# Kernel tuning notes

Hardware: AMD Instinct MI355X
Metric: run time of the kernel (lower is better)

Reference implementation:

```python
import jax, jax.numpy as jnp
import numpy as np

EMBED_DIM = 1024
NUM_HEADS = 16
HEAD_DIM = EMBED_DIM // NUM_HEADS
B, S = 4, 2048


def setup_inputs() -> dict:
    key = jax.random.key(0)
    ks = jax.random.split(key, 9)
    scale = 1.0 / np.sqrt(EMBED_DIM)
    inp = {
        "inputs": jax.random.normal(ks[0], (B, S, EMBED_DIM), dtype=jnp.float32),
        "rotation_params": jax.random.normal(ks[1], (B, S, EMBED_DIM), dtype=jnp.float32),
        "entangle_params": jax.random.normal(ks[2], (B, S, EMBED_DIM), dtype=jnp.float32),
        # Linear weights stored as (out, in) like torch; applied as x @ W.T
        "Wq": jax.random.normal(ks[3], (EMBED_DIM, EMBED_DIM), dtype=jnp.float32) * scale,
        "Wk": jax.random.normal(ks[4], (EMBED_DIM, EMBED_DIM), dtype=jnp.float32) * scale,
        "Wv": jax.random.normal(ks[5], (EMBED_DIM, EMBED_DIM), dtype=jnp.float32) * scale,
        "Wrot": jax.random.normal(ks[6], (EMBED_DIM, EMBED_DIM), dtype=jnp.float32) * scale,
        "Went": jax.random.normal(ks[7], (EMBED_DIM, EMBED_DIM), dtype=jnp.float32) * scale,
        "Wo": jax.random.normal(ks[8], (EMBED_DIM, EMBED_DIM), dtype=jnp.float32) * scale,
    }
    return inp


def _split_heads(x):
    b, s, e = x.shape
    return x.reshape(b, s, NUM_HEADS, HEAD_DIM).transpose(0, 2, 1, 3)  # (B,H,S,D)


def reference(inputs, rotation_params, entangle_params, Wq, Wk, Wv, Wrot, Went, Wo):
    Q = inputs @ Wq.T + rotation_params @ Wrot.T
    K = inputs @ Wk.T + entangle_params @ Went.T
    V = inputs @ Wv.T
    Qh, Kh, Vh = _split_heads(Q), _split_heads(K), _split_heads(V)
    scores = jnp.einsum("bhqd,bhkd->bhqk", Qh, Kh) / jnp.sqrt(jnp.float32(HEAD_DIM))
    attn = jax.nn.softmax(scores, axis=-1)  # dropout p=0 -> identity
    out = jnp.einsum("bhqk,bhkd->bhqd", attn, Vh)
    out = out.transpose(0, 2, 1, 3).reshape(inputs.shape[0], inputs.shape[1], EMBED_DIM)
    return out @ Wo.T
```

## Files before the change

### kernel.cpp

```cpp
#include <hip/hip_runtime.h>
#include <stdint.h>


typedef unsigned short u16;
typedef __bf16 bf16x8 __attribute__((ext_vector_type(8)));
typedef float f32x4 __attribute__((ext_vector_type(4)));
typedef float f32x16 __attribute__((ext_vector_type(16)));
typedef uint32_t u32x4 __attribute__((ext_vector_type(4)));

#define MFMA_BF16(a, b, c) __builtin_amdgcn_mfma_f32_16x16x32_bf16((a), (b), (c), 0, 0, 0)
#define MFMA32(a, b, c)    __builtin_amdgcn_mfma_f32_32x32x16_bf16((a), (b), (c), 0, 0, 0)
#define GAMMA 0.18033688011112042f
#define BHSTRIDE 131072
#define FENCE() __builtin_amdgcn_sched_barrier(0)

static __device__ __forceinline__ u16 f2bf(float f) {
    uint32_t u = __builtin_bit_cast(uint32_t, f);
    u = (u + 0x7FFFu + ((u >> 16) & 1u)) >> 16;
    return (u16)u;
}

static __device__ __forceinline__ uint32_t pk_rne2(float a, float b) {
    uint32_t ua = __builtin_bit_cast(uint32_t, a);
    uint32_t ub = __builtin_bit_cast(uint32_t, b);
    ua += 0x7FFFu + ((ua >> 16) & 1u);
    ub += 0x7FFFu + ((ub >> 16) & 1u);
    return __builtin_amdgcn_perm(ub, ua, 0x07060302);
}

static __device__ __forceinline__ void async_copy16(const void* g, void* l) {
    __builtin_amdgcn_global_load_lds((__attribute__((address_space(1))) void*)g,
                                     (__attribute__((address_space(3))) void*)l,
                                     16, 0, 0);
}

static __device__ __forceinline__ float aexp2(float x) {
    float r;
    asm("v_exp_f32 %0, %1" : "=v"(r) : "v"(x));
    return r;
}

static __device__ __forceinline__ uint32_t cvtpk(float a, float b) {
    uint32_t r;
    asm("v_cvt_pk_bf16_f32 %0, %1, %2" : "=v"(r) : "v"(a), "v"(b));
    return r;
}

static __device__ __forceinline__ void plswap(uint32_t& a, uint32_t& b) {
    asm("v_permlane32_swap_b32 %0, %1" : "+v"(a), "+v"(b));
}

static __device__ __forceinline__ bf16x8 mkfrag(uint32_t w0, uint32_t w1,
                                                uint32_t w2, uint32_t w3) {
    u32x4 u = {w0, w1, w2, w3};
    return __builtin_bit_cast(bf16x8, u);
}

struct CvtArgs { const float* s[6]; u16* d[6]; };

__global__ __launch_bounds__(256) void cvt_kernel(CvtArgs a, int nelem) {
    const float* s = a.s[blockIdx.z];
    u16* d = a.d[blockIdx.z];
    int i = (blockIdx.x * 256 + threadIdx.x) * 8;
    float4 f0 = *(const float4*)(s + i);
    float4 f1 = *(const float4*)(s + i + 4);
    uint4 w;
    w.x = pk_rne2(f0.x, f0.y); w.y = pk_rne2(f0.z, f0.w);
    w.z = pk_rne2(f1.x, f1.y); w.w = pk_rne2(f1.z, f1.w);
    *(uint4*)(d + i) = w;
}

__global__ __launch_bounds__(256, 3) void qk_proj(
    const u16* __restrict__ Xb,
    const u16* __restrict__ Wqb, const u16* __restrict__ RVb,
    const u16* __restrict__ Wrotb, u16* __restrict__ Qhm,
    const u16* __restrict__ Wkb, const u16* __restrict__ EOb,
    const u16* __restrict__ Wentb, u16* __restrict__ Khm)
{
    __shared__ __align__(16) u16 lA[128 * 64];
    __shared__ __align__(16) u16 lB[128 * 64];

    const int tid  = threadIdx.x;
    const int lane = tid & 63;
    const int wave = tid >> 6;
    const int wm   = (wave >> 1) * 64;
    const int wn   = (wave & 1) * 64;
    const size_t m0 = (size_t)blockIdx.x * 128;

    const bool isK = blockIdx.y >= 8;
    const size_t n0 = (size_t)(blockIdx.y & 7) * 128;
    const u16* A0 = Xb;
    const u16* W0 = isK ? Wkb  : Wqb;
    const u16* A1 = isK ? EOb  : RVb;
    const u16* W1 = isK ? Wentb : Wrotb;
    u16*       C  = isK ? Khm  : Qhm;
    const float scale = isK ? 1.0f : GAMMA;

    const int row8 = tid >> 3;
    const int cp   = tid & 7;
    const int fr   = lane & 15;
    const int g    = lane >> 4;

    f32x4 acc[4][4] = {};

    for (int p = 0; p < 2; ++p) {
        const u16* A = p ? A1 : A0;
        const u16* W = p ? W1 : W0;
        for (int k0 = 0; k0 < 1024; k0 += 64) {
            __syncthreads();
#pragma unroll
            for (int it = 0; it < 4; ++it) {
                int row = it * 32 + row8;
                int sc = cp ^ (((row >> 3) ^ row) & 7);
                async_copy16(A + ((m0 + row) * 1024 + k0 + sc * 8),
                             (char*)lA + it * 4096 + tid * 16);
                async_copy16(W + ((n0 + row) * 1024 + k0 + sc * 8),
                             (char*)lB + it * 4096 + tid * 16);
            }
            __syncthreads();

            bf16x8 af[4][2], bfm[4][2];
#pragma unroll
            for (int i = 0; i < 4; ++i) {
                int row = wm + i * 16 + fr;
                int sw = ((row >> 3) ^ row) & 7;
                af[i][0] = *(const bf16x8*)(lA + row * 64 + (g ^ sw) * 8);
                af[i][1] = *(const bf16x8*)(lA + row * 64 + ((4 + g) ^ sw) * 8);
            }
#pragma unroll
            for (int j = 0; j < 4; ++j) {
                int row = wn + j * 16 + fr;
                int sw = ((row >> 3) ^ row) & 7;
                bfm[j][0] = *(const bf16x8*)(lB + row * 64 + (g ^ sw) * 8);
                bfm[j][1] = *(const bf16x8*)(lB + row * 64 + ((4 + g) ^ sw) * 8);
            }
#pragma unroll
            for (int i = 0; i < 4; ++i)
#pragma unroll
                for (int j = 0; j < 4; ++j) {
                    acc[i][j] = MFMA_BF16(af[i][0], bfm[j][0], acc[i][j]);
                    acc[i][j] = MFMA_BF16(af[i][1], bfm[j][1], acc[i][j]);
                }
        }
    }

#pragma unroll
    for (int i = 0; i < 4; ++i)
#pragma unroll
        for (int j = 0; j < 4; ++j)
#pragma unroll
            for (int rg = 0; rg < 4; ++rg) {
                size_t row = m0 + wm + i * 16 + g * 4 + rg;
                size_t col = n0 + wn + j * 16 + fr;
                size_t addr = ((row >> 11) * 16 + (col >> 6)) * BHSTRIDE
                            + (row & 2047) * 64 + (col & 63);
                C[addr] = f2bf(acc[i][j][rg] * scale);
            }
}

template <int AMODE, int CMODE>
__global__ __launch_bounds__(256, 2) void gemm_bt(
    const u16* __restrict__ A0, const u16* __restrict__ W0,
    const u16* __restrict__ A1, const u16* __restrict__ W1,
    void* __restrict__ Cv, int K, int npairs, float scale)
{
    __shared__ __align__(16) u16 lA[128 * 64];
    __shared__ __align__(16) u16 lB[128 * 64];

    const int tid  = threadIdx.x;
    const int lane = tid & 63;
    const int wave = tid >> 6;
    const int wm   = (wave >> 1) * 64;
    const int wn   = (wave & 1) * 64;
    const size_t m0 = (size_t)blockIdx.x * 128;
    const size_t n0 = (size_t)blockIdx.y * 128;

    const int row8 = tid >> 3;
    const int cp   = tid & 7;
    const int fr   = lane & 15;
    const int g    = lane >> 4;

    const size_t bb = (m0 >> 11) * 16;
    const size_t s0 = m0 & 2047;

    f32x4 acc[4][4] = {};

    for (int p = 0; p < npairs; ++p) {
        const u16* A = p ? A1 : A0;
        const u16* W = p ? W1 : W0;
        for (int k0 = 0; k0 < K; k0 += 64) {
            __syncthreads();
#pragma unroll
            for (int it = 0; it < 4; ++it) {
                int row = it * 32 + row8;
                int sc = cp ^ (((row >> 3) ^ row) & 7);
                if (AMODE == 0) {
                    async_copy16(A + ((m0 + row) * (size_t)K + k0 + sc * 8),
                                 (char*)lA + it * 4096 + tid * 16);
                } else {
                    size_t base = (bb + (size_t)(k0 >> 6)) * BHSTRIDE;
                    async_copy16(A + base + (s0 + row) * 64 + sc * 8,
                                 (char*)lA + it * 4096 + tid * 16);
                }
                async_copy16(W + ((n0 + row) * (size_t)K + k0 + sc * 8),
                             (char*)lB + it * 4096 + tid * 16);
            }
            __syncthreads();

            bf16x8 af[4][2], bfm[4][2];
#pragma unroll
            for (int i = 0; i < 4; ++i) {
                int row = wm + i * 16 + fr;
                int sw = ((row >> 3) ^ row) & 7;
                af[i][0] = *(const bf16x8*)(lA + row * 64 + (g ^ sw) * 8);
                af[i][1] = *(const bf16x8*)(lA + row * 64 + ((4 + g) ^ sw) * 8);
            }
#pragma unroll
            for (int j = 0; j < 4; ++j) {
                int row = wn + j * 16 + fr;
                int sw = ((row >> 3) ^ row) & 7;
                bfm[j][0] = *(const bf16x8*)(lB + row * 64 + (g ^ sw) * 8);
                bfm[j][1] = *(const bf16x8*)(lB + row * 64 + ((4 + g) ^ sw) * 8);
            }
#pragma unroll
            for (int i = 0; i < 4; ++i)
#pragma unroll
                for (int j = 0; j < 4; ++j) {
                    acc[i][j] = MFMA_BF16(af[i][0], bfm[j][0], acc[i][j]);
                    acc[i][j] = MFMA_BF16(af[i][1], bfm[j][1], acc[i][j]);
                }
        }
    }

#pragma unroll
    for (int i = 0; i < 4; ++i)
#pragma unroll
        for (int j = 0; j < 4; ++j) {
            if (CMODE == 2) {
                size_t row0 = m0 + wm + i * 16 + g * 4;
                size_t col  = n0 + wn + j * 16 + fr;
                size_t addr = ((row0 >> 11) * 16 + (col >> 6)) * BHSTRIDE
                            + (size_t)(col & 63) * 2048 + (row0 & 2047);
                ushort4 pk;
                pk.x = f2bf(acc[i][j][0] * scale);
                pk.y = f2bf(acc[i][j][1] * scale);
                pk.z = f2bf(acc[i][j][2] * scale);
                pk.w = f2bf(acc[i][j][3] * scale);
                *(ushort4*)((u16*)Cv + addr) = pk;
            } else {
#pragma unroll
                for (int rg = 0; rg < 4; ++rg) {
                    size_t row = m0 + wm + i * 16 + g * 4 + rg;
                    size_t col = n0 + wn + j * 16 + fr;
                    float v = acc[i][j][rg] * scale;
                    if (CMODE == 0) {
                        ((float*)Cv)[row * 1024 + col] = v;
                    } else {
                        size_t addr = ((row >> 11) * 16 + (col >> 6)) * BHSTRIDE
                                    + (row & 2047) * 64 + (col & 63);
                        ((u16*)Cv)[addr] = f2bf(v);
                    }
                }
            }
        }
}

__global__ __launch_bounds__(256, 2) void flash_kernel(
    const u16* __restrict__ Qhm, const u16* __restrict__ Khm,
    const u16* __restrict__ Vt, u16* __restrict__ Ohm)
{
    __shared__ __align__(16) u16 sK[2][128 * 64];
    __shared__ __align__(16) u16 sVt[2][64 * 128];

    const int tid  = threadIdx.x;
    const int lane = tid & 63;
    const int wave = tid >> 6;
    const int l31  = lane & 31;
    const int hg   = lane >> 5;

    const int lin  = blockIdx.x;
    const int slot = lin >> 3;
    const int bh   = (lin & 7) + 8 * (slot >> 3);
    const int q0   = (slot & 7) * 256;

    const u16* Qh = Qhm + (size_t)bh * BHSTRIDE;
    const u16* Kh = Khm + (size_t)bh * BHSTRIDE;
    const u16* Vh = Vt  + (size_t)bh * BHSTRIDE;
    u16*       Oh = Ohm + (size_t)bh * BHSTRIDE;

    bf16x8 qbf[2][4];
#pragma unroll
    for (int qt = 0; qt < 2; ++qt)
#pragma unroll
        for (int dc = 0; dc < 4; ++dc)
            qbf[qt][dc] = *(const bf16x8*)(Qh +
                (size_t)(q0 + wave * 64 + qt * 32 + l31) * 64 + dc * 16 + hg * 8);

    f32x16 oaccA[2] = {};
    f32x16 oaccB[2] = {};
    float lsA[2] = {}, lsB[2] = {};

    const int krow8 = tid >> 3, kcp = tid & 7;
    const int vd16  = tid >> 4, vcp = tid & 15;

    auto stage = [&](int buf, int kt) {
#pragma unroll
        for (int it = 0; it < 4; ++it) {
            int row = it * 32 + krow8;
            int sc = kcp ^ (((row >> 3) ^ row) & 7);
            async_copy16(Kh + (size_t)(kt * 128 + row) * 64 + sc * 8,
                         (char*)(&sK[buf][0]) + it * 4096 + tid * 16);
        }
#pragma unroll
        for (int it = 0; it < 4; ++it) {
            int d = it * 16 + vd16;
            int sc = vcp ^ (d & 15);
            async_copy16(Vh + (size_t)d * 2048 + kt * 128 + sc * 8,
                         (char*)(&sVt[buf][0]) + it * 4096 + tid * 16);
        }
    };

    auto qk2 = [&](const u16* sKc, int kc, f32x16& sa0, f32x16& sa1) {
        sa0 = (f32x16){};
        sa1 = (f32x16){};
        const int krow = kc * 32 + l31;
        const int ksw = ((krow >> 3) ^ krow) & 7;
#pragma unroll
        for (int dc = 0; dc < 4; ++dc) {
            bf16x8 ka = *(const bf16x8*)(sKc + krow * 64 + ((dc * 2 + hg) ^ ksw) * 8);
            sa0 = MFMA32(ka, qbf[0][dc], sa0);
            sa1 = MFMA32(ka, qbf[1][dc], sa1);
        }
    };

    auto sm = [&](const f32x16& sa, bf16x8& o0, bf16x8& o1, float* ls) {
        float p[16];
#pragma unroll
        for (int r = 0; r < 16; ++r) p[r] = aexp2(sa[r]);
#pragma unroll
        for (int r = 0; r < 16; ++r) ls[r & 1] += p[r];
        uint32_t w0 = cvtpk(p[0],  p[1]),  w1 = cvtpk(p[2],  p[3]);
        uint32_t w2 = cvtpk(p[4],  p[5]),  w3 = cvtpk(p[6],  p[7]);
        uint32_t w4 = cvtpk(p[8],  p[9]),  w5 = cvtpk(p[10], p[11]);
        uint32_t w6 = cvtpk(p[12], p[13]), w7 = cvtpk(p[14], p[15]);
        plswap(w0, w2); plswap(w1, w3);
        plswap(w4, w6); plswap(w5, w7);
        o0 = mkfrag(w0, w1, w2, w3);
        o1 = mkfrag(w4, w5, w6, w7);
    };

    auto pv2 = [&](const u16* sVc, int kc, bf16x8 a0, bf16x8 a1,
                   bf16x8 b0, bf16x8 b1) {
        bf16x8 vb[2][2];
#pragma unroll
        for (int sub = 0; sub < 2; ++sub)
#pragma unroll
            for (int dt = 0; dt < 2; ++dt) {
                int dr = dt * 32 + l31;
                vb[sub][dt] = *(const bf16x8*)(sVc + dr * 128 +
                    ((kc * 4 + sub * 2 + hg) ^ (dr & 15)) * 8);
            }
        oaccA[0] = MFMA32(a0, vb[0][0], oaccA[0]);
        oaccA[1] = MFMA32(a0, vb[0][1], oaccA[1]);
        oaccB[0] = MFMA32(b0, vb[0][0], oaccB[0]);
        oaccB[1] = MFMA32(b0, vb[0][1], oaccB[1]);
        oaccA[0] = MFMA32(a1, vb[1][0], oaccA[0]);
        oaccA[1] = MFMA32(a1, vb[1][1], oaccA[1]);
        oaccB[0] = MFMA32(b1, vb[1][0], oaccB[0]);
        oaccB[1] = MFMA32(b1, vb[1][1], oaccB[1]);
    };

    stage(0, 0);
    __syncthreads();

    int cur = 0;
    for (int kt = 0; kt < 16; ++kt) {
        const u16* sKc = &sK[cur][0];
        const u16* sVc = &sVt[cur][0];

        f32x16 sA, sB, nA, nB;
        qk2(sKc, 0, sA, sB);
        if (kt < 15) stage(cur ^ 1, kt + 1);
        FENCE();

        bf16x8 a0, a1, b0, b1;
        sm(sA, a0, a1, lsA);   FENCE();
        qk2(sKc, 1, nA, nB);   FENCE();
        sm(sB, b0, b1, lsB);   FENCE();
        pv2(sVc, 0, a0, a1, b0, b1); FENCE();
        sm(nA, a0, a1, lsA);   FENCE();
        qk2(sKc, 2, sA, sB);   FENCE();
        sm(nB, b0, b1, lsB);   FENCE();
        pv2(sVc, 1, a0, a1, b0, b1); FENCE();
        sm(sA, a0, a1, lsA);   FENCE();
        qk2(sKc, 3, nA, nB);   FENCE();
        sm(sB, b0, b1, lsB);   FENCE();
        pv2(sVc, 2, a0, a1, b0, b1); FENCE();
        sm(nA, a0, a1, lsA);   FENCE();
        sm(nB, b0, b1, lsB);   FENCE();
        pv2(sVc, 3, a0, a1, b0, b1);

        __syncthreads();
        cur ^= 1;
    }

#pragma unroll
    for (int qt = 0; qt < 2; ++qt) {
        float l = qt ? (lsB[0] + lsB[1]) : (lsA[0] + lsA[1]);
        l += __shfl_xor(l, 32);
        float inv = 1.0f / l;
        const f32x16* oa = qt ? oaccB : oaccA;
#pragma unroll
        for (int r = 0; r < 16; ++r) {
            int row = (r & 3) + 4 * hg + 8 * (r >> 2);
            float invr = __shfl(inv, row);
            size_t grow = (size_t)q0 + wave * 64 + qt * 32 + row;
            Oh[grow * 64 + l31]      = f2bf(oa[0][r] * invr);
            Oh[grow * 64 + 32 + l31] = f2bf(oa[1][r] * invr);
        }
    }
}

extern "C" void kernel_launch(void* const* d_in, const int* in_sizes, int n_in,
                              void* d_out, int out_size, void* d_ws, size_t ws_size,
                              hipStream_t stream)
{
    const float* X    = (const float*)d_in[0];
    const float* R    = (const float*)d_in[1];
    const float* E    = (const float*)d_in[2];
    const float* Wq   = (const float*)d_in[3];
    const float* Wk   = (const float*)d_in[4];
    const float* Wv   = (const float*)d_in[5];
    const float* Wrot = (const float*)d_in[6];
    const float* Went = (const float*)d_in[7];
    const float* Wo   = (const float*)d_in[8];

    const size_t NT = 8192 * 1024;
    const size_t NW = 1024 * 1024;

    u16* Qhm = (u16*)d_out;
    u16* Khm = Qhm + NT;
    u16* Xb  = (u16*)d_ws;
    u16* RVb = Xb + NT;
    u16* EOb = RVb + NT;
    u16* Wqb = EOb + NT;
    u16* Wkb   = Wqb + NW;
    u16* Wvb   = Wkb + NW;
    u16* Wrotb = Wvb + NW;
    u16* Wentb = Wrotb + NW;
    u16* Wob   = Wentb + NW;

    {
        CvtArgs a{};
        a.s[0] = X; a.s[1] = R; a.s[2] = E;
        a.d[0] = Xb; a.d[1] = RVb; a.d[2] = EOb;
        cvt_kernel<<<dim3(4096, 1, 3), 256, 0, stream>>>(a, (int)NT);
    }
    {
        CvtArgs a{};
        a.s[0] = Wq; a.s[1] = Wk; a.s[2] = Wv; a.s[3] = Wrot; a.s[4] = Went; a.s[5] = Wo;
        a.d[0] = Wqb; a.d[1] = Wkb; a.d[2] = Wvb; a.d[3] = Wrotb; a.d[4] = Wentb; a.d[5] = Wob;
        cvt_kernel<<<dim3(512, 1, 6), 256, 0, stream>>>(a, (int)NW);
    }

    qk_proj<<<dim3(64, 16), 256, 0, stream>>>(Xb, Wqb, RVb, Wrotb, Qhm,
                                              Wkb, EOb, Wentb, Khm);
    gemm_bt<0, 2><<<dim3(64, 8), 256, 0, stream>>>(Xb, Wvb, nullptr, nullptr,
                                                   RVb, 1024, 1, 1.0f);
    flash_kernel<<<dim3(512), 256, 0, stream>>>(Qhm, Khm, RVb, EOb);
    gemm_bt<1, 0><<<dim3(64, 8), 256, 0, stream>>>(EOb, Wob, nullptr, nullptr,
                                                   d_out, 1024, 1, 1.0f);
}
```

Measured before the change: 364.1 us.

## Fuse V projection into QK projection kernel and merge conversion launches

Merges the two fp32-to-bf16 conversion launches into a single 9-slice launch, where weight slices exit early past their size. Adds a qkv_proj kernel that computes Q, K and V projections in one grid of 64x24 blocks, writing V transposed into a separate workspace region. The new path runs only when the workspace is large enough, so V no longer overwrites RVb. This removes launch overhead and tail gaps between kernels, at the cost of load imbalance because V blocks do half the K-loop work.

```diff
diff --git a/kernel.cpp b/kernel.cpp
--- a/kernel.cpp
+++ b/kernel.cpp
@@ -56,9 +56,10 @@
     return __builtin_bit_cast(bf16x8, u);
 }
 
-struct CvtArgs { const float* s[6]; u16* d[6]; };
-
-__global__ __launch_bounds__(256) void cvt_kernel(CvtArgs a, int nelem) {
+struct CvtArgs { const float* s[9]; u16* d[9]; };
+
+__global__ __launch_bounds__(256) void cvt_kernel(CvtArgs a) {
+    if (blockIdx.z >= 3 && blockIdx.x >= 512) return;
     const float* s = a.s[blockIdx.z];
     u16* d = a.d[blockIdx.z];
     int i = (blockIdx.x * 256 + threadIdx.x) * 8;
@@ -70,6 +71,113 @@
     *(uint4*)(d + i) = w;
 }
 
+__global__ __launch_bounds__(256, 3) void qkv_proj(
+    const u16* __restrict__ Xb,
+    const u16* __restrict__ Wqb, const u16* __restrict__ RVb,
+    const u16* __restrict__ Wrotb, u16* __restrict__ Qhm,
+    const u16* __restrict__ Wkb, const u16* __restrict__ EOb,
+    const u16* __restrict__ Wentb, u16* __restrict__ Khm,
+    const u16* __restrict__ Wvb, u16* __restrict__ Vt)
+{
+    __shared__ __align__(16) u16 lA[128 * 64];
+    __shared__ __align__(16) u16 lB[128 * 64];
+
+    const int tid  = threadIdx.x;
+    const int lane = tid & 63;
+    const int wave = tid >> 6;
+    const int wm   = (wave >> 1) * 64;
+    const int wn   = (wave & 1) * 64;
+    const size_t m0 = (size_t)blockIdx.x * 128;
+
+    const int sel = blockIdx.y >> 3;
+    const size_t n0 = (size_t)(blockIdx.y & 7) * 128;
+    const u16* W0 = sel == 0 ? Wqb : (sel == 1 ? Wkb : Wvb);
+    const u16* A1 = sel == 1 ? EOb : RVb;
+    const u16* W1 = sel == 1 ? Wentb : Wrotb;
+    const float scale = sel == 0 ? GAMMA : 1.0f;
+    const int npairs = sel == 2 ? 1 : 2;
+
+    const int row8 = tid >> 3;
+    const int cp   = tid & 7;
+    const int fr   = lane & 15;
+    const int g    = lane >> 4;
+
+    f32x4 acc[4][4] = {};
+
+    for (int p = 0; p < npairs; ++p) {
+        const u16* A = p ? A1 : Xb;
+        const u16* W = p ? W1 : W0;
+        for (int k0 = 0; k0 < 1024; k0 += 64) {
+            __syncthreads();
+#pragma unroll
+            for (int it = 0; it < 4; ++it) {
+                int row = it * 32 + row8;
+                int sc = cp ^ (((row >> 3) ^ row) & 7);
+                async_copy16(A + ((m0 + row) * 1024 + k0 + sc * 8),
+                             (char*)lA + it * 4096 + tid * 16);
+                async_copy16(W + ((n0 + row) * 1024 + k0 + sc * 8),
+                             (char*)lB + it * 4096 + tid * 16);
+            }
+            __syncthreads();
+
+            bf16x8 af[4][2], bfm[4][2];
+#pragma unroll
+            for (int i = 0; i < 4; ++i) {
+                int row = wm + i * 16 + fr;
+                int sw = ((row >> 3) ^ row) & 7;
+                af[i][0] = *(const bf16x8*)(lA + row * 64 + (g ^ sw) * 8);
+                af[i][1] = *(const bf16x8*)(lA + row * 64 + ((4 + g) ^ sw) * 8);
+            }
+#pragma unroll
+            for (int j = 0; j < 4; ++j) {
+                int row = wn + j * 16 + fr;
+                int sw = ((row >> 3) ^ row) & 7;
+                bfm[j][0] = *(const bf16x8*)(lB + row * 64 + (g ^ sw) * 8);
+                bfm[j][1] = *(const bf16x8*)(lB + row * 64 + ((4 + g) ^ sw) * 8);
+            }
+#pragma unroll
+            for (int i = 0; i < 4; ++i)
+#pragma unroll
+                for (int j = 0; j < 4; ++j) {
+                    acc[i][j] = MFMA_BF16(af[i][0], bfm[j][0], acc[i][j]);
+                    acc[i][j] = MFMA_BF16(af[i][1], bfm[j][1], acc[i][j]);
+                }
+        }
+    }
+
+    if (sel == 2) {
+#pragma unroll
+        for (int i = 0; i < 4; ++i)
+#pragma unroll
+            for (int j = 0; j < 4; ++j) {
+                size_t row0 = m0 + wm + i * 16 + g * 4;
+                size_t col  = n0 + wn + j * 16 + fr;
+                size_t addr = ((row0 >> 11) * 16 + (col >> 6)) * BHSTRIDE
+                            + (size_t)(col & 63) * 2048 + (row0 & 2047);
+                ushort4 pk;
+                pk.x = f2bf(acc[i][j][0]);
+                pk.y = f2bf(acc[i][j][1]);
+                pk.z = f2bf(acc[i][j][2]);
+                pk.w = f2bf(acc[i][j][3]);
+                *(ushort4*)(Vt + addr) = pk;
+            }
+    } else {
+        u16* C = sel == 0 ? Qhm : Khm;
+#pragma unroll
+        for (int i = 0; i < 4; ++i)
+#pragma unroll
+            for (int j = 0; j < 4; ++j)
+#pragma unroll
+                for (int rg = 0; rg < 4; ++rg) {
+                    size_t row = m0 + wm + i * 16 + g * 4 + rg;
+                    size_t col = n0 + wn + j * 16 + fr;
+                    size_t addr = ((row >> 11) * 16 + (col >> 6)) * BHSTRIDE
+                                + (row & 2047) * 64 + (col & 63);
+                    C[addr] = f2bf(acc[i][j][rg] * scale);
+                }
+    }
+}
+
 __global__ __launch_bounds__(256, 3) void qk_proj(
     const u16* __restrict__ Xb,
     const u16* __restrict__ Wqb, const u16* __restrict__ RVb,
@@ -89,7 +197,6 @@
 
     const bool isK = blockIdx.y >= 8;
     const size_t n0 = (size_t)(blockIdx.y & 7) * 128;
-    const u16* A0 = Xb;
     const u16* W0 = isK ? Wkb  : Wqb;
     const u16* A1 = isK ? EOb  : RVb;
     const u16* W1 = isK ? Wentb : Wrotb;
@@ -104,7 +211,7 @@
     f32x4 acc[4][4] = {};
 
     for (int p = 0; p < 2; ++p) {
-        const u16* A = p ? A1 : A0;
+        const u16* A = p ? A1 : Xb;
         const u16* W = p ? W1 : W0;
         for (int k0 = 0; k0 < 1024; k0 += 64) {
             __syncthreads();
@@ -449,25 +556,33 @@
     u16* Wrotb = Wvb + NW;
     u16* Wentb = Wrotb + NW;
     u16* Wob   = Wentb + NW;
+    u16* VtX   = Wob + NW;
+
+    const bool bigws = ws_size >= (4 * NT + 6 * NW) * sizeof(u16);
+    u16* Vt = bigws ? VtX : RVb;
 
     {
         CvtArgs a{};
-        a.s[0] = X; a.s[1] = R; a.s[2] = E;
-        a.d[0] = Xb; a.d[1] = RVb; a.d[2] = EOb;
-        cvt_kernel<<<dim3(4096, 1, 3), 256, 0, stream>>>(a, (int)NT);
-    }
-    {
-        CvtArgs a{};
-        a.s[0] = Wq; a.s[1] = Wk; a.s[2] = Wv; a.s[3] = Wrot; a.s[4] = Went; a.s[5] = Wo;
-        a.d[0] = Wqb; a.d[1] = Wkb; a.d[2] = Wvb; a.d[3] = Wrotb; a.d[4] = Wentb; a.d[5] = Wob;
-        cvt_kernel<<<dim3(512, 1, 6), 256, 0, stream>>>(a, (int)NW);
-    }
-
-    qk_proj<<<dim3(64, 16), 256, 0, stream>>>(Xb, Wqb, RVb, Wrotb, Qhm,
-                                              Wkb, EOb, Wentb, Khm);
-    gemm_bt<0, 2><<<dim3(64, 8), 256, 0, stream>>>(Xb, Wvb, nullptr, nullptr,
-                                                   RVb, 1024, 1, 1.0f);
-    flash_kernel<<<dim3(512), 256, 0, stream>>>(Qhm, Khm, RVb, EOb);
+        a.s[0] = X;  a.s[1] = R;  a.s[2] = E;
+        a.s[3] = Wq; a.s[4] = Wk; a.s[5] = Wv;
+        a.s[6] = Wrot; a.s[7] = Went; a.s[8] = Wo;
+        a.d[0] = Xb;  a.d[1] = RVb;  a.d[2] = EOb;
+        a.d[3] = Wqb; a.d[4] = Wkb;  a.d[5] = Wvb;
+        a.d[6] = Wrotb; a.d[7] = Wentb; a.d[8] = Wob;
+        cvt_kernel<<<dim3(4096, 1, 9), 256, 0, stream>>>(a);
+    }
+
+    if (bigws) {
+        qkv_proj<<<dim3(64, 24), 256, 0, stream>>>(Xb, Wqb, RVb, Wrotb, Qhm,
+                                                   Wkb, EOb, Wentb, Khm,
+                                                   Wvb, VtX);
+    } else {
+        qk_proj<<<dim3(64, 16), 256, 0, stream>>>(Xb, Wqb, RVb, Wrotb, Qhm,
+                                                  Wkb, EOb, Wentb, Khm);
+        gemm_bt<0, 2><<<dim3(64, 8), 256, 0, stream>>>(Xb, Wvb, nullptr, nullptr,
+                                                       RVb, 1024, 1, 1.0f);
+    }
+    flash_kernel<<<dim3(512), 256, 0, stream>>>(Qhm, Khm, Vt, EOb);
     gemm_bt<1, 0><<<dim3(64, 8), 256, 0, stream>>>(EOb, Wob, nullptr, nullptr,
                                                    d_out, 1024, 1, 1.0f);
 }
```

After: 336.8 us. 1.08x faster.
